# Optimization experiments

Measured on AMD Instinct MI355X. Metric: run time of the kernel, lower is better.

The kernel has to match this reference:

```python
import jax, jax.numpy as jnp
import numpy as np

D_MODEL = 1024
NUM_HEADS = 16
HEAD_DIM = D_MODEL // NUM_HEADS


def setup_inputs() -> dict:
    key = jax.random.key(0)
    ks = jax.random.split(key, 6)
    B, S = 2, 2048
    w_scale = 1.0 / np.sqrt(D_MODEL)  # keep logits O(1) so the naive exp-softmax is stable
    return {
        "x": jax.random.normal(ks[0], (B, S, D_MODEL), dtype=jnp.float32),
        "y": jax.random.normal(ks[1], (B, S, D_MODEL), dtype=jnp.float32),
        "mask": jnp.zeros((S, S), dtype=jnp.float32),
        "Wq": jax.random.normal(ks[2], (D_MODEL, D_MODEL), dtype=jnp.float32) * w_scale,
        "Wk": jax.random.normal(ks[3], (D_MODEL, D_MODEL), dtype=jnp.float32) * w_scale,
        "Wv": jax.random.normal(ks[4], (D_MODEL, D_MODEL), dtype=jnp.float32) * w_scale,
        "Wo": jax.random.normal(ks[5], (D_MODEL, D_MODEL), dtype=jnp.float32) * w_scale,
    }


def _naive_softmax(s):
    # faithful to nirmalya_softmax: plain exp, sum + eps, no max subtraction
    p1 = jnp.exp(s)
    p2 = jnp.sum(p1, axis=-1, keepdims=True) + 1e-10
    return p1 / p2


def reference(x, y, mask, Wq, Wk, Wv, Wo):
    B, S, _ = x.shape
    # nn.Linear(bias=False): t @ W.T ; split heads -> [B, H, S, Dh]
    def split_heads(t):
        return t.reshape(B, S, NUM_HEADS, HEAD_DIM).transpose(0, 2, 1, 3)

    k = split_heads(x @ Wk.T)
    v = split_heads(x @ Wv.T)
    q = split_heads(y @ Wq.T)

    scores = jnp.einsum("bhqd,bhkd->bhqk", q, k) / np.sqrt(HEAD_DIM)
    scores = scores + mask  # [S,S] broadcasts over [B,H,S,S] (same math as permute-add-permute)
    attn = _naive_softmax(scores)
    out = jnp.einsum("bhqk,bhkd->bhqd", attn, v)  # [B,H,S,Dh]
    out = out.transpose(0, 2, 1, 3).reshape(B, S, D_MODEL)
    return out @ Wo.T
```

## Files before the change

kernel.cpp:

```cpp
#include <hip/hip_runtime.h>
#include <stdint.h>

typedef unsigned short u16;
typedef __attribute__((ext_vector_type(4))) float f32x4;
typedef __attribute__((ext_vector_type(2))) __bf16 bf16x2;
typedef __attribute__((ext_vector_type(8))) __bf16 bf16x8;
typedef __attribute__((ext_vector_type(4))) u16 u16x4;
typedef __attribute__((ext_vector_type(2))) _Float16 f16x2;
typedef __attribute__((ext_vector_type(4))) _Float16 f16x4;

#define AS1 __attribute__((address_space(1)))
#define AS3 __attribute__((address_space(3)))
#define GLOAD_LDS16(gp, lp) \
  __builtin_amdgcn_global_load_lds((const AS1 void*)(gp), (AS3 void*)(lp), 16, 0, 0)

__device__ __forceinline__ u16 f2bf(float f) {
  union { float f; unsigned u; } v; v.f = f;
  return (u16)((v.u + 0x7FFFu + ((v.u >> 16) & 1u)) >> 16);
}
__device__ __forceinline__ u16 f2h(float f) {
  union { _Float16 h; u16 u; } v; v.h = (_Float16)f; return v.u;
}
__device__ __forceinline__ float bf2f(u16 u) {
  union { unsigned u; float f; } v; v.u = ((unsigned)u) << 16; return v.f;
}
__device__ __forceinline__ float fexp2(float x) {
#if __has_builtin(__builtin_amdgcn_exp2f)
  return __builtin_amdgcn_exp2f(x);
#else
  return exp2f(x);
#endif
}
__device__ __forceinline__ f16x2 pkf16(float a, float b) {
#if __has_builtin(__builtin_amdgcn_cvt_pkrtz)
  return __builtin_bit_cast(f16x2, __builtin_amdgcn_cvt_pkrtz(a, b));
#else
  f16x2 r; r.x = (_Float16)a; r.y = (_Float16)b; return r;
#endif
}
__device__ __forceinline__ u16x4 pack4(float a, float b, float c, float d) {
#if __has_builtin(__builtin_amdgcn_cvt_pk_bf16_f32)
  union { struct { bf16x2 lo, hi; } p; u16x4 v; } u;
  u.p.lo = __builtin_amdgcn_cvt_pk_bf16_f32(a, b);
  u.p.hi = __builtin_amdgcn_cvt_pk_bf16_f32(c, d);
  return u.v;
#else
  u16x4 r; r.x = f2bf(a); r.y = f2bf(b); r.z = f2bf(c); r.w = f2bf(d); return r;
#endif
}

#define LOG2E 1.44269504f

__global__ __launch_bounds__(256) void convert_all(
    const float* __restrict__ x, const float* __restrict__ y,
    const float* __restrict__ wq, const float* __restrict__ wk,
    const float* __restrict__ wv, const float* __restrict__ wo,
    const float* __restrict__ mask,
    u16* __restrict__ xb, u16* __restrict__ yb, u16* __restrict__ wqb,
    u16* __restrict__ wkb, u16* __restrict__ wvb, u16* __restrict__ wob,
    u16* __restrict__ maskb) {
  size_t i = (size_t)blockIdx.x * 256 + threadIdx.x;
  const float* src; u16* dst; float scale = 1.0f; size_t off;
  if (i < (size_t)(1u << 20)) { src = x; dst = xb; off = i; }
  else if (i < (size_t)(2u << 20)) { src = y; dst = yb; off = i - (1u << 20); }
  else if (i < (size_t)(3u << 20)) {
    size_t j = i - (size_t)(2u << 20);
    unsigned w = (unsigned)(j >> 18); off = j & ((1u << 18) - 1);
    if (w == 0)      { src = wq; dst = wqb; scale = 0.125f * LOG2E; }
    else if (w == 1) { src = wk; dst = wkb; }
    else if (w == 2) { src = wv; dst = wvb; }
    else             { src = wo; dst = wob; }
  } else { src = mask; dst = maskb; scale = LOG2E; off = i - (size_t)(3u << 20); }
  f32x4 v = ((const f32x4*)src)[off];
  ((u16x4*)dst)[off] = pack4(v.x * scale, v.y * scale, v.z * scale, v.w * scale);
}

__device__ __forceinline__ void gemm_core64(
    const u16* __restrict__ A, const u16* __restrict__ Bt, int tm, int tn,
    u16* As, u16* Bs, f32x4 acc[4][4], int wave, int lane) {
  constexpr int K = 1024;
  const int l15 = lane & 15, quad = lane >> 4;
  const int wr = wave >> 1, wc = wave & 1;
  const int srow = lane >> 3;
  const int scol = ((lane & 7) ^ (srow & 7)) * 8;
  const u16* Ag = A + (size_t)(tm + wave * 32 + srow) * K + scol;
  const u16* Bg = Bt + (size_t)(tn + wave * 32 + srow) * K + scol;
  const int rsw = l15 & 7;

  for (int k0 = 0; k0 < K; k0 += 64) {
    __syncthreads();
#pragma unroll
    for (int c = 0; c < 4; ++c)
      GLOAD_LDS16(Ag + (size_t)c * 8 * K + k0, &As[(wave * 4 + c) * 512]);
#pragma unroll
    for (int c = 0; c < 4; ++c)
      GLOAD_LDS16(Bg + (size_t)c * 8 * K + k0, &Bs[(wave * 4 + c) * 512]);
    __syncthreads();
#pragma unroll
    for (int kq = 0; kq < 2; ++kq) {
      bf16x8 af[4], bfr[4];
#pragma unroll
      for (int mi = 0; mi < 4; ++mi)
        af[mi] = *(const bf16x8*)&As[(wr * 64 + mi * 16 + l15) * 64 +
                                     ((kq * 4 + quad) ^ rsw) * 8];
#pragma unroll
      for (int ni = 0; ni < 4; ++ni)
        bfr[ni] = *(const bf16x8*)&Bs[(wc * 64 + ni * 16 + l15) * 64 +
                                      ((kq * 4 + quad) ^ rsw) * 8];
#pragma unroll
      for (int mi = 0; mi < 4; ++mi)
#pragma unroll
        for (int ni = 0; ni < 4; ++ni)
          acc[mi][ni] = __builtin_amdgcn_mfma_f32_16x16x32_bf16(
              af[mi], bfr[ni], acc[mi][ni], 0, 0, 0);
    }
  }
}

__global__ __launch_bounds__(256, 3) void qkv_gemm(
    const u16* __restrict__ xb, const u16* __restrict__ yb,
    const u16* __restrict__ wqb, const u16* __restrict__ wkb,
    const u16* __restrict__ wvb,
    u16* __restrict__ Qw, u16* __restrict__ Kw, u16* __restrict__ Vtw) {
  __shared__ __align__(16) u16 As[128 * 64];
  __shared__ __align__(16) u16 Bs[128 * 64];
  const int tid = threadIdx.x, wave = tid >> 6, lane = tid & 63;
  const int l15 = lane & 15, quad = lane >> 4;
  const int wr = wave >> 1, wc = wave & 1;
  const int z = blockIdx.z;
  const u16 *A, *Bt; int tm, tn;
  if (z == 0)      { A = yb;  Bt = wqb; tm = blockIdx.y * 128; tn = blockIdx.x * 128; }
  else if (z == 1) { A = xb;  Bt = wkb; tm = blockIdx.y * 128; tn = blockIdx.x * 128; }
  else             { A = wvb; Bt = xb;  tm = blockIdx.x * 128; tn = blockIdx.y * 128; }

  f32x4 acc[4][4] = {};
  gemm_core64(A, Bt, tm, tn, As, Bs, acc, wave, lane);

#pragma unroll
  for (int mi = 0; mi < 4; ++mi) {
#pragma unroll
    for (int ni = 0; ni < 4; ++ni) {
#pragma unroll
      for (int r = 0; r < 4; ++r) {
        int gm = tm + wr * 64 + mi * 16 + quad * 4 + r;
        int gn = tn + wc * 64 + ni * 16 + l15;
        float val = acc[mi][ni][r];
        if (z == 2) {
          int h = gm >> 6, dh = gm & 63, b = gn >> 11, s = gn & 2047;
          Vtw[(((size_t)(b * 16 + h) * 64 + dh) << 11) + s] = f2h(val);
        } else {
          int b = gm >> 11, s = gm & 2047, h = gn >> 6, dh = gn & 63;
          u16* dst = (z == 0) ? Qw : Kw;
          dst[(((size_t)(b * 16 + h) * 2048 + s) << 6) + dh] = f2bf(val);
        }
      }
    }
  }
}

__global__ __launch_bounds__(256, 3) void out_gemm(
    const u16* __restrict__ Ow, const u16* __restrict__ wob,
    float* __restrict__ C) {
  constexpr int K = 1024;
  __shared__ __align__(16) u16 As[64 * 64];
  __shared__ __align__(16) u16 Bs[128 * 64];
  const int tid = threadIdx.x, wave = tid >> 6, lane = tid & 63;
  const int l15 = lane & 15, quad = lane >> 4;
  const int wr = wave >> 1, wc = wave & 1;
  const int tm = blockIdx.y * 64, tn = blockIdx.x * 128;
  const int srow = lane >> 3;
  const int scol = ((lane & 7) ^ (srow & 7)) * 8;
  const u16* Ag = Ow + (size_t)(tm + wave * 16 + srow) * K + scol;
  const u16* Bg = wob + (size_t)(tn + wave * 32 + srow) * K + scol;
  const int rsw = l15 & 7;

  f32x4 acc[2][4] = {};
  for (int k0 = 0; k0 < K; k0 += 64) {
    __syncthreads();
#pragma unroll
    for (int c = 0; c < 2; ++c)
      GLOAD_LDS16(Ag + (size_t)c * 8 * K + k0, &As[(wave * 2 + c) * 512]);
#pragma unroll
    for (int c = 0; c < 4; ++c)
      GLOAD_LDS16(Bg + (size_t)c * 8 * K + k0, &Bs[(wave * 4 + c) * 512]);
    __syncthreads();
#pragma unroll
    for (int kq = 0; kq < 2; ++kq) {
      bf16x8 af[2], bfr[4];
#pragma unroll
      for (int mi = 0; mi < 2; ++mi)
        af[mi] = *(const bf16x8*)&As[(wr * 32 + mi * 16 + l15) * 64 +
                                     ((kq * 4 + quad) ^ rsw) * 8];
#pragma unroll
      for (int ni = 0; ni < 4; ++ni)
        bfr[ni] = *(const bf16x8*)&Bs[(wc * 64 + ni * 16 + l15) * 64 +
                                      ((kq * 4 + quad) ^ rsw) * 8];
#pragma unroll
      for (int mi = 0; mi < 2; ++mi)
#pragma unroll
        for (int ni = 0; ni < 4; ++ni)
          acc[mi][ni] = __builtin_amdgcn_mfma_f32_16x16x32_bf16(
              af[mi], bfr[ni], acc[mi][ni], 0, 0, 0);
    }
  }

#pragma unroll
  for (int mi = 0; mi < 2; ++mi)
#pragma unroll
    for (int ni = 0; ni < 4; ++ni)
#pragma unroll
      for (int r = 0; r < 4; ++r) {
        int gm = tm + wr * 32 + mi * 16 + quad * 4 + r;
        int gn = tn + wc * 64 + ni * 16 + l15;
        C[(size_t)gm * 1024 + gn] = acc[mi][ni][r];
      }
}

__global__ __launch_bounds__(256, 3) void attn_kernel(
    const u16* __restrict__ Qw, const u16* __restrict__ Kw,
    const u16* __restrict__ Vtw, const u16* __restrict__ maskb,
    u16* __restrict__ Ow) {
  constexpr int S = 2048;
  __shared__ __align__(16) u16 Ks[128 * 64];
  __shared__ __align__(16) u16 Vs[64 * 128];
  const int tid = threadIdx.x;
  const int wave = tid >> 6, lane = tid & 63;
  const int l15 = lane & 15, quad = lane >> 4;
  const int qt = blockIdx.x, h = blockIdx.y, b = blockIdx.z;
  const size_t head = ((size_t)(b * 16 + h)) * S * 64;
  const int qbase = qt * 128 + wave * 32;

  bf16x8 qf[2][2];
#pragma unroll
  for (int q2 = 0; q2 < 2; ++q2)
#pragma unroll
    for (int kq = 0; kq < 2; ++kq)
      qf[q2][kq] = *(const bf16x8*)&Qw[head +
          (size_t)(qbase + q2 * 16 + l15) * 64 + kq * 32 + quad * 8];

  const _Float16 one_h = (_Float16)1.0f;
  const f16x4 ones = {one_h, one_h, one_h, one_h};

  f32x4 oa[2][4] = {};
  f32x4 den[2] = {};

  const int k_r = lane >> 3;
  const int k_c = ((lane & 7) ^ k_r) * 8;
  const int v_r = lane >> 4;
  const int v_cl = lane & 15;
  const int rsw = l15 & 7;

  for (int kt = 0; kt < S; kt += 128) {
    __syncthreads();
#pragma unroll
    for (int c = 0; c < 4; ++c) {
      int g = wave * 4 + c;
      GLOAD_LDS16(&Kw[head + (size_t)(kt + g * 8 + k_r) * 64 + k_c], &Ks[g * 512]);
    }
#pragma unroll
    for (int c = 0; c < 4; ++c) {
      int g = wave * 4 + c;
      int dh = g * 4 + v_r;
      GLOAD_LDS16(&Vtw[head + (size_t)dh * S + kt + ((v_cl ^ (dh & 15)) * 8)],
                  &Vs[g * 512]);
    }
    u16x4 mq[2][8];
#pragma unroll
    for (int q2 = 0; q2 < 2; ++q2)
#pragma unroll
      for (int mk = 0; mk < 8; ++mk)
        mq[q2][mk] = *(const u16x4*)&maskb[(size_t)(qbase + q2 * 16 + l15) * S +
                                           kt + mk * 16 + quad * 4];
    __syncthreads();

#pragma unroll
    for (int mk = 0; mk < 8; ++mk) {
      f32x4 sa[2] = {};
#pragma unroll
      for (int kq = 0; kq < 2; ++kq) {
        bf16x8 ak = *(const bf16x8*)&Ks[(mk * 16 + l15) * 64 +
                                        ((kq * 4 + quad) ^ rsw) * 8];
        sa[0] = __builtin_amdgcn_mfma_f32_16x16x32_bf16(ak, qf[0][kq], sa[0], 0, 0, 0);
        sa[1] = __builtin_amdgcn_mfma_f32_16x16x32_bf16(ak, qf[1][kq], sa[1], 0, 0, 0);
      }
      f16x4 pf[2];
#pragma unroll
      for (int q2 = 0; q2 < 2; ++q2) {
        float p0 = fexp2(sa[q2][0] + bf2f(mq[q2][mk].x));
        float p1 = fexp2(sa[q2][1] + bf2f(mq[q2][mk].y));
        float p2 = fexp2(sa[q2][2] + bf2f(mq[q2][mk].z));
        float p3 = fexp2(sa[q2][3] + bf2f(mq[q2][mk].w));
        union { struct { f16x2 lo, hi; } p; f16x4 v; } u;
        u.p.lo = pkf16(p0, p1); u.p.hi = pkf16(p2, p3);
        pf[q2] = u.v;
      }
#pragma unroll
      for (int nv = 0; nv < 4; ++nv) {
        f16x4 bv = *(const f16x4*)&Vs[(nv * 16 + l15) * 128 +
                                      ((mk * 2 + (quad >> 1)) ^ l15) * 8 +
                                      (quad & 1) * 4];
        oa[0][nv] = __builtin_amdgcn_mfma_f32_16x16x16f16(pf[0], bv, oa[0][nv], 0, 0, 0);
        oa[1][nv] = __builtin_amdgcn_mfma_f32_16x16x16f16(pf[1], bv, oa[1][nv], 0, 0, 0);
      }
      den[0] = __builtin_amdgcn_mfma_f32_16x16x16f16(pf[0], ones, den[0], 0, 0, 0);
      den[1] = __builtin_amdgcn_mfma_f32_16x16x16f16(pf[1], ones, den[1], 0, 0, 0);
    }
  }

#pragma unroll
  for (int q2 = 0; q2 < 2; ++q2) {
#pragma unroll
    for (int nv = 0; nv < 4; ++nv) {
#pragma unroll
      for (int r = 0; r < 4; ++r) {
        int srow = qbase + q2 * 16 + quad * 4 + r;
        int dh = nv * 16 + l15;
        float val = oa[q2][nv][r] / (den[q2][r] + 1e-10f);
        Ow[((size_t)(b * S + srow) << 10) + h * 64 + dh] = f2bf(val);
      }
    }
  }
}

extern "C" void kernel_launch(void* const* d_in, const int* in_sizes, int n_in,
                              void* d_out, int out_size, void* d_ws, size_t ws_size,
                              hipStream_t stream) {
  const float* x    = (const float*)d_in[0];
  const float* y    = (const float*)d_in[1];
  const float* mask = (const float*)d_in[2];
  const float* Wq   = (const float*)d_in[3];
  const float* Wk   = (const float*)d_in[4];
  const float* Wv   = (const float*)d_in[5];
  const float* Wo   = (const float*)d_in[6];
  char* ws = (char*)d_ws;
  const size_t MB = (size_t)1 << 20;
  u16* xb  = (u16*)(ws + 0  * MB);
  u16* yb  = (u16*)(ws + 8  * MB);
  u16* wqb = (u16*)(ws + 16 * MB);
  u16* wkb = (u16*)(ws + 18 * MB);
  u16* wvb = (u16*)(ws + 20 * MB);
  u16* wob = (u16*)(ws + 22 * MB);
  u16* Qw  = (u16*)(ws + 24 * MB);
  u16* Kw  = (u16*)(ws + 32 * MB);
  u16* Vtw = (u16*)(ws + 40 * MB);
  u16* Ow  = (u16*)(ws + 48 * MB);
  u16* maskb = (u16*)(ws + 56 * MB);

  convert_all<<<16384, 256, 0, stream>>>(x, y, Wq, Wk, Wv, Wo, mask,
                                         xb, yb, wqb, wkb, wvb, wob, maskb);
  qkv_gemm<<<dim3(8, 32, 3), 256, 0, stream>>>(xb, yb, wqb, wkb, wvb, Qw, Kw, Vtw);
  attn_kernel<<<dim3(16, 16, 2), 256, 0, stream>>>(Qw, Kw, Vtw, maskb, Ow);
  out_gemm<<<dim3(8, 64), 256, 0, stream>>>(Ow, wob, (float*)d_out);
  (void)in_sizes; (void)n_in; (void)out_size; (void)ws_size;
}
```

Measured before the change: 233.7 us.

## Split attention over key halves, use 16x16x32 f16 MFMA, add combine kernel

The attention kernel now splits the key dimension into two halves across the grid z axis, doubling the number of blocks from 512 to 1024. Each half writes unnormalized fp32 partial outputs and row denominators, and a new combine kernel sums them, normalizes and packs to bf16. The PV product moves from 16x16x16 to 16x16x32 f16 MFMA by reordering key rows and changing the LDS swizzle, and occupancy is raised to 4 blocks per SM. The cost is the extra partial-output traffic (two fp32 copies, reusing workspace and the output buffer) and one more kernel launch.

```diff
diff --git a/kernel.cpp b/kernel.cpp
--- a/kernel.cpp
+++ b/kernel.cpp
@@ -6,8 +6,8 @@
 typedef __attribute__((ext_vector_type(2))) __bf16 bf16x2;
 typedef __attribute__((ext_vector_type(8))) __bf16 bf16x8;
 typedef __attribute__((ext_vector_type(4))) u16 u16x4;
-typedef __attribute__((ext_vector_type(2))) _Float16 f16x2;
-typedef __attribute__((ext_vector_type(4))) _Float16 f16x4;
+typedef __attribute__((ext_vector_type(2))) __fp16 h16x2;
+typedef __attribute__((ext_vector_type(8))) __fp16 h16x8;
 
 #define AS1 __attribute__((address_space(1)))
 #define AS3 __attribute__((address_space(3)))
@@ -31,12 +31,8 @@
   return exp2f(x);
 #endif
 }
-__device__ __forceinline__ f16x2 pkf16(float a, float b) {
-#if __has_builtin(__builtin_amdgcn_cvt_pkrtz)
-  return __builtin_bit_cast(f16x2, __builtin_amdgcn_cvt_pkrtz(a, b));
-#else
-  f16x2 r; r.x = (_Float16)a; r.y = (_Float16)b; return r;
-#endif
+__device__ __forceinline__ h16x2 pkh(float a, float b) {
+  return __builtin_amdgcn_cvt_pkrtz(a, b);
 }
 __device__ __forceinline__ u16x4 pack4(float a, float b, float c, float d) {
 #if __has_builtin(__builtin_amdgcn_cvt_pk_bf16_f32)
@@ -216,18 +212,20 @@
       }
 }
 
-__global__ __launch_bounds__(256, 3) void attn_kernel(
+__global__ __launch_bounds__(256, 4) void attn_kernel(
     const u16* __restrict__ Qw, const u16* __restrict__ Kw,
     const u16* __restrict__ Vtw, const u16* __restrict__ maskb,
-    u16* __restrict__ Ow) {
+    float* __restrict__ Op0, float* __restrict__ Op1, float* __restrict__ denb) {
   constexpr int S = 2048;
   __shared__ __align__(16) u16 Ks[128 * 64];
   __shared__ __align__(16) u16 Vs[64 * 128];
   const int tid = threadIdx.x;
   const int wave = tid >> 6, lane = tid & 63;
   const int l15 = lane & 15, quad = lane >> 4;
-  const int qt = blockIdx.x, h = blockIdx.y, b = blockIdx.z;
+  const int qt = blockIdx.x, h = blockIdx.y, z = blockIdx.z;
+  const int b = z >> 1, ks = z & 1;
   const size_t head = ((size_t)(b * 16 + h)) * S * 64;
+  const int kbase = ks * 1024;
   const int qbase = qt * 128 + wave * 32;
 
   bf16x8 qf[2][2];
@@ -238,88 +236,124 @@
       qf[q2][kq] = *(const bf16x8*)&Qw[head +
           (size_t)(qbase + q2 * 16 + l15) * 64 + kq * 32 + quad * 8];
 
-  const _Float16 one_h = (_Float16)1.0f;
-  const f16x4 ones = {one_h, one_h, one_h, one_h};
+  const __fp16 one_h = (__fp16)1.0f;
+  const h16x8 ones = {one_h, one_h, one_h, one_h, one_h, one_h, one_h, one_h};
 
   f32x4 oa[2][4] = {};
   f32x4 den[2] = {};
 
   const int k_r = lane >> 3;
-  const int k_c = ((lane & 7) ^ k_r) * 8;
   const int v_r = lane >> 4;
   const int v_cl = lane & 15;
-  const int rsw = l15 & 7;
-
-  for (int kt = 0; kt < S; kt += 128) {
+  const int rswz = (l15 & 3) | (((l15 >> 2) & 1) << 2);
+
+  for (int kt = 0; kt < 1024; kt += 128) {
     __syncthreads();
 #pragma unroll
     for (int c = 0; c < 4; ++c) {
       int g = wave * 4 + c;
-      GLOAD_LDS16(&Kw[head + (size_t)(kt + g * 8 + k_r) * 64 + k_c], &Ks[g * 512]);
+      int swz = (k_r & 3) | ((g & 1) << 2);
+      int k_c = ((lane & 7) ^ swz) * 8;
+      GLOAD_LDS16(&Kw[head + (size_t)(kbase + kt + g * 8 + k_r) * 64 + k_c],
+                  &Ks[g * 512]);
     }
 #pragma unroll
     for (int c = 0; c < 4; ++c) {
       int g = wave * 4 + c;
       int dh = g * 4 + v_r;
-      GLOAD_LDS16(&Vtw[head + (size_t)dh * S + kt + ((v_cl ^ (dh & 15)) * 8)],
+      GLOAD_LDS16(&Vtw[head + (size_t)dh * S + kbase + kt + ((v_cl ^ (dh & 15)) * 8)],
                   &Vs[g * 512]);
     }
-    u16x4 mq[2][8];
+    u16x4 mq[2][4][2];
 #pragma unroll
     for (int q2 = 0; q2 < 2; ++q2)
 #pragma unroll
-      for (int mk = 0; mk < 8; ++mk)
-        mq[q2][mk] = *(const u16x4*)&maskb[(size_t)(qbase + q2 * 16 + l15) * S +
-                                           kt + mk * 16 + quad * 4];
-    __syncthreads();
-
-#pragma unroll
-    for (int mk = 0; mk < 8; ++mk) {
-      f32x4 sa[2] = {};
-#pragma unroll
-      for (int kq = 0; kq < 2; ++kq) {
-        bf16x8 ak = *(const bf16x8*)&Ks[(mk * 16 + l15) * 64 +
-                                        ((kq * 4 + quad) ^ rsw) * 8];
-        sa[0] = __builtin_amdgcn_mfma_f32_16x16x32_bf16(ak, qf[0][kq], sa[0], 0, 0, 0);
-        sa[1] = __builtin_amdgcn_mfma_f32_16x16x32_bf16(ak, qf[1][kq], sa[1], 0, 0, 0);
-      }
-      f16x4 pf[2];
+      for (int t = 0; t < 4; ++t)
+#pragma unroll
+        for (int s = 0; s < 2; ++s)
+          mq[q2][t][s] = *(const u16x4*)&maskb[(size_t)(qbase + q2 * 16 + l15) * S +
+                                               kbase + kt + t * 32 + quad * 8 + s * 4];
+    __syncthreads();
+
+#pragma unroll
+    for (int t = 0; t < 4; ++t) {
+      f32x4 sa[2][2] = {};
+#pragma unroll
+      for (int s = 0; s < 2; ++s) {
+        int krow = t * 32 + ((l15 >> 2) << 3) + s * 4 + (l15 & 3);
+#pragma unroll
+        for (int kq = 0; kq < 2; ++kq) {
+          bf16x8 ak = *(const bf16x8*)&Ks[krow * 64 + ((kq * 4 + quad) ^ rswz) * 8];
+          sa[s][0] = __builtin_amdgcn_mfma_f32_16x16x32_bf16(ak, qf[0][kq], sa[s][0], 0, 0, 0);
+          sa[s][1] = __builtin_amdgcn_mfma_f32_16x16x32_bf16(ak, qf[1][kq], sa[s][1], 0, 0, 0);
+        }
+      }
+      h16x8 pf[2];
 #pragma unroll
       for (int q2 = 0; q2 < 2; ++q2) {
-        float p0 = fexp2(sa[q2][0] + bf2f(mq[q2][mk].x));
-        float p1 = fexp2(sa[q2][1] + bf2f(mq[q2][mk].y));
-        float p2 = fexp2(sa[q2][2] + bf2f(mq[q2][mk].z));
-        float p3 = fexp2(sa[q2][3] + bf2f(mq[q2][mk].w));
-        union { struct { f16x2 lo, hi; } p; f16x4 v; } u;
-        u.p.lo = pkf16(p0, p1); u.p.hi = pkf16(p2, p3);
+        union { h16x2 p[4]; h16x8 v; } u;
+#pragma unroll
+        for (int s = 0; s < 2; ++s) {
+          float e0 = fexp2(sa[s][q2][0] + bf2f(mq[q2][t][s].x));
+          float e1 = fexp2(sa[s][q2][1] + bf2f(mq[q2][t][s].y));
+          float e2 = fexp2(sa[s][q2][2] + bf2f(mq[q2][t][s].z));
+          float e3 = fexp2(sa[s][q2][3] + bf2f(mq[q2][t][s].w));
+          u.p[s * 2 + 0] = pkh(e0, e1);
+          u.p[s * 2 + 1] = pkh(e2, e3);
+        }
         pf[q2] = u.v;
       }
 #pragma unroll
       for (int nv = 0; nv < 4; ++nv) {
-        f16x4 bv = *(const f16x4*)&Vs[(nv * 16 + l15) * 128 +
-                                      ((mk * 2 + (quad >> 1)) ^ l15) * 8 +
-                                      (quad & 1) * 4];
-        oa[0][nv] = __builtin_amdgcn_mfma_f32_16x16x16f16(pf[0], bv, oa[0][nv], 0, 0, 0);
-        oa[1][nv] = __builtin_amdgcn_mfma_f32_16x16x16f16(pf[1], bv, oa[1][nv], 0, 0, 0);
-      }
-      den[0] = __builtin_amdgcn_mfma_f32_16x16x16f16(pf[0], ones, den[0], 0, 0, 0);
-      den[1] = __builtin_amdgcn_mfma_f32_16x16x16f16(pf[1], ones, den[1], 0, 0, 0);
-    }
-  }
-
+        h16x8 bv = *(const h16x8*)&Vs[(nv * 16 + l15) * 128 +
+                                      (((t * 4 + quad) ^ l15) * 8)];
+        oa[0][nv] = __builtin_amdgcn_mfma_f32_16x16x32_f16(pf[0], bv, oa[0][nv], 0, 0, 0);
+        oa[1][nv] = __builtin_amdgcn_mfma_f32_16x16x32_f16(pf[1], bv, oa[1][nv], 0, 0, 0);
+      }
+      den[0] = __builtin_amdgcn_mfma_f32_16x16x32_f16(pf[0], ones, den[0], 0, 0, 0);
+      den[1] = __builtin_amdgcn_mfma_f32_16x16x32_f16(pf[1], ones, den[1], 0, 0, 0);
+    }
+  }
+
+  float* Op = ks ? Op1 : Op0;
 #pragma unroll
   for (int q2 = 0; q2 < 2; ++q2) {
 #pragma unroll
     for (int nv = 0; nv < 4; ++nv) {
 #pragma unroll
       for (int r = 0; r < 4; ++r) {
-        int srow = qbase + q2 * 16 + quad * 4 + r;
+        int q = qbase + q2 * 16 + quad * 4 + r;
         int dh = nv * 16 + l15;
-        float val = oa[q2][nv][r] / (den[q2][r] + 1e-10f);
-        Ow[((size_t)(b * S + srow) << 10) + h * 64 + dh] = f2bf(val);
-      }
-    }
-  }
+        Op[((size_t)(b * S + q) << 10) + h * 64 + dh] = oa[q2][nv][r];
+      }
+    }
+  }
+  if (l15 == 0) {
+#pragma unroll
+    for (int q2 = 0; q2 < 2; ++q2)
+#pragma unroll
+      for (int r = 0; r < 4; ++r) {
+        int q = qbase + q2 * 16 + quad * 4 + r;
+        denb[((size_t)(ks * 2 + b) * 16 + h) * 2048 + q] = den[q2][r];
+      }
+  }
+}
+
+__global__ __launch_bounds__(256) void combine(
+    const float* __restrict__ Op0, const float* __restrict__ Op1,
+    const float* __restrict__ denb, u16* __restrict__ Ow) {
+  size_t i = (size_t)blockIdx.x * 256 + threadIdx.x;
+  size_t flat = i * 4;
+  int c = (int)(flat & 1023), h = c >> 6;
+  int s = (int)((flat >> 10) & 2047);
+  int b = (int)(flat >> 21);
+  f32x4 a = ((const f32x4*)Op0)[i];
+  f32x4 d = ((const f32x4*)Op1)[i];
+  float dn = denb[((size_t)b * 16 + h) * 2048 + s] +
+             denb[((size_t)(2 + b) * 16 + h) * 2048 + s] + 1e-10f;
+  float r = 1.0f / dn;
+  ((u16x4*)Ow)[i] = pack4((a.x + d.x) * r, (a.y + d.y) * r,
+                          (a.z + d.z) * r, (a.w + d.w) * r);
 }
 
 extern "C" void kernel_launch(void* const* d_in, const int* in_sizes, int n_in,
@@ -345,11 +379,15 @@
   u16* Vtw = (u16*)(ws + 40 * MB);
   u16* Ow  = (u16*)(ws + 48 * MB);
   u16* maskb = (u16*)(ws + 56 * MB);
+  float* Op0  = (float*)(ws + 0 * MB);
+  float* Op1  = (float*)d_out;
+  float* denb = (float*)(ws + 16 * MB);
 
   convert_all<<<16384, 256, 0, stream>>>(x, y, Wq, Wk, Wv, Wo, mask,
                                          xb, yb, wqb, wkb, wvb, wob, maskb);
   qkv_gemm<<<dim3(8, 32, 3), 256, 0, stream>>>(xb, yb, wqb, wkb, wvb, Qw, Kw, Vtw);
-  attn_kernel<<<dim3(16, 16, 2), 256, 0, stream>>>(Qw, Kw, Vtw, maskb, Ow);
+  attn_kernel<<<dim3(16, 16, 4), 256, 0, stream>>>(Qw, Kw, Vtw, maskb, Op0, Op1, denb);
+  combine<<<4096, 256, 0, stream>>>(Op0, Op1, denb, Ow);
   out_gemm<<<dim3(8, 64), 256, 0, stream>>>(Ow, wob, (float*)d_out);
   (void)in_sizes; (void)n_in; (void)out_size; (void)ws_size;
 }
```

Result: slower. 245.7 us (+5.1%).
